# Kernel tuning notes

Hardware: AMD Instinct MI355X
Metric: run time of the kernel (lower is better)

## Reference

```python
import jax, jax.numpy as jnp
import numpy as np

HEADS = 8

def setup_inputs() -> dict:
    key = jax.random.key(0)
    ks = jax.random.split(key, 4)
    b, n, d = 4, 4097, 128  # n = 64*64 + 1 (CLS + spatial)
    x = jax.random.normal(ks[0], (b, n, d), dtype=jnp.float32)
    W_qkv = jax.random.normal(ks[1], (d, 3 * d), dtype=jnp.float32) * (d ** -0.5)
    b_qkv = jnp.zeros((3 * d,), dtype=jnp.float32)
    W_out = jax.random.normal(ks[2], (d, d), dtype=jnp.float32) * (d ** -0.5)
    b_out = jnp.zeros((d,), dtype=jnp.float32)
    return {"x": x, "W_qkv": W_qkv, "b_qkv": b_qkv, "W_out": W_out, "b_out": b_out}

def reference(x, W_qkv, b_qkv, W_out, b_out):
    b, n, d = x.shape
    h = HEADS
    dh = d // h
    scale = d ** -0.5  # note: module scales by dim**-0.5, not head_dim**-0.5
    qkv = x @ W_qkv + b_qkv                      # [b, n, 3d]
    q, k, v = jnp.split(qkv, 3, axis=-1)
    def to_heads(t):
        return t.reshape(b, n, h, dh).transpose(0, 2, 1, 3)  # [b, h, n, dh]
    q, k, v = to_heads(q), to_heads(k), to_heads(v)
    dots = jnp.einsum('bhid,bhjd->bhij', q, k) * scale       # [b, h, n, n]
    attn = jax.nn.softmax(dots, axis=-1)
    out = jnp.einsum('bhij,bhjd->bhid', attn, v)             # [b, h, n, dh]
    out = out.transpose(0, 2, 1, 3).reshape(b, n, d)
    return out @ W_out + b_out
```

## Files before the change

### kernel.cpp

```cpp
#include <hip/hip_runtime.h>
#include <hip/hip_bf16.h>
#include <stdint.h>


#define BB 4
#define NN 4097
#define NNP 4112
#define DD 128
#define HH 8
#define DH 16
#define BH (BB*HH)
#define ROWS (BB*NN)

typedef _Float16 h4 __attribute__((ext_vector_type(4)));
typedef _Float16 h8 __attribute__((ext_vector_type(8)));
typedef __fp16   fp16v2 __attribute__((ext_vector_type(2)));
typedef float    f4 __attribute__((ext_vector_type(4)));

#if __has_builtin(__builtin_amdgcn_exp2f)
#define EXP2F(x) __builtin_amdgcn_exp2f(x)
#else
#define EXP2F(x) exp2f(x)
#endif

union H4u { h4 v; fp16v2 p[2]; };

static __device__ __forceinline__ H4u pack4u(float a, float b, float c, float d) {
    H4u u;
#if __has_builtin(__builtin_amdgcn_cvt_pkrtz)
    u.p[0] = __builtin_amdgcn_cvt_pkrtz(a, b);
    u.p[1] = __builtin_amdgcn_cvt_pkrtz(c, d);
#else
    u.v[0] = (_Float16)a; u.v[1] = (_Float16)b; u.v[2] = (_Float16)c; u.v[3] = (_Float16)d;
#endif
    return u;
}

__global__ __launch_bounds__(384) void qkv_proj(
    const float* __restrict__ x,
    const float* __restrict__ Wqkv,
    const float* __restrict__ bqkv,
    _Float16* __restrict__ Qh,
    _Float16* __restrict__ Kh,
    _Float16* __restrict__ Vh)
{
    const int t  = threadIdx.x;
    const int r0 = blockIdx.x * 4;

    const float bias = bqkv[t];
    float acc0 = bias, acc1 = bias, acc2 = bias, acc3 = bias;

    const float* x0 = x + (size_t)r0 * DD;
    #pragma unroll 4
    for (int k = 0; k < DD; ++k) {
        const float w = Wqkv[k*384 + t];
        acc0 += x0[k]        * w;
        acc1 += x0[DD + k]   * w;
        acc2 += x0[2*DD + k] * w;
        acc3 += x0[3*DD + k] * w;
    }

    const int which = t >> 7, c = t & 127, head = c >> 4, i = c & 15;
    const float QSCALE = 0.08838834764831845f * 1.4426950408889634f;
    _Float16* base = (which == 0) ? Qh : ((which == 1) ? Kh : Vh);
    const float mul = (which == 0) ? QSCALE : 1.0f;

    float accs[4] = {acc0, acc1, acc2, acc3};
    #pragma unroll
    for (int r = 0; r < 4; ++r) {
        const int row  = r0 + r;
        const int bidx = row / NN;
        const int nrow = row - bidx*NN;
        base[(((size_t)(bidx*HH + head))*NNP + nrow)*DH + i] = (_Float16)(accs[r] * mul);
    }
}

__global__ __launch_bounds__(256) void vt_transpose(
    const _Float16* __restrict__ Vh,
    _Float16* __restrict__ Vt)
{
    __shared__ _Float16 tile[128][DH + 2];
    const int tl  = blockIdx.x;
    const int bh  = blockIdx.y;
    const int tid = threadIdx.x;
    const int n0  = tl * 128;
    const int rem = (n0 + 128 <= NNP) ? 128 : (NNP - n0);

    {
        const int r  = tid >> 1;
        const int i8 = (tid & 1) * 8;
        const int rc = (r < rem) ? r : (rem - 1);
        const h8 v = *(const h8*)(Vh + ((size_t)bh*NNP + n0 + rc)*DH + i8);
        #pragma unroll
        for (int j = 0; j < 8; ++j) tile[r][i8 + j] = v[j];
    }
    __syncthreads();
    {
        const int i    = tid >> 4;
        const int nseg = tid & 15;
        if (nseg * 8 < rem) {
            h8 v;
            #pragma unroll
            for (int j = 0; j < 8; ++j) v[j] = tile[nseg*8 + j][i];
            *(h8*)(Vt + ((size_t)bh*DH + i)*NNP + n0 + nseg*8) = v;
        }
    }
}

__global__ __launch_bounds__(256, 8) void attn_mfma(
    const _Float16* __restrict__ Qh,
    const _Float16* __restrict__ Kh,
    const _Float16* __restrict__ Vt,
    _Float16* __restrict__ PACC,
    float* __restrict__ PL)
{
    const int qt   = blockIdx.x;
    const int bh   = blockIdx.y;
    const int sp   = blockIdx.z;
    const int tid  = threadIdx.x;
    const int wave = tid >> 6;
    const int lane = tid & 63;
    const int quad = lane >> 4;
    const int l16  = lane & 15;
    const int bidx = bh >> 3, head = bh & 7;

    const int qbase = qt*256 + wave*64;

    const _Float16* Qb = Qh + (size_t)bh*NNP*DH;
    h4 qf[4];
    #pragma unroll
    for (int g = 0; g < 4; ++g) {
        const int qr = qbase + g*16 + l16;
        const int qc = (qr < NN) ? qr : (NN-1);
        qf[g] = *(const h4*)(Qb + (size_t)qc*DH + quad*4);
    }

    f4 acc[4] = {{0,0,0,0},{0,0,0,0},{0,0,0,0},{0,0,0,0}};
    float ls[4] = {0.f,0.f,0.f,0.f};

    const int t0 = sp*64;
    const int t1 = t0 + 64;

    const _Float16* kp = Kh + ((size_t)bh*NNP + (size_t)t0*16 + l16)*DH + quad*4;
    const _Float16* vp = Vt + ((size_t)bh*DH + l16)*NNP + t0*16 + quad*4;

    h4 ak = *(const h4*)kp;
    h4 av = *(const h4*)vp;
    const f4 zero = {0.f,0.f,0.f,0.f};
#if __has_builtin(__builtin_amdgcn_fdot2)
    const fp16v2 one2 = {(__fp16)1.0f, (__fp16)1.0f};
#endif

    for (int tt = t0; tt < t1; ++tt) {
        kp += 16*DH; vp += 16;
        const h4 nak = *(const h4*)kp;
        const h4 nav = *(const h4*)vp;
        #pragma unroll
        for (int g = 0; g < 4; ++g) {
            f4 d = __builtin_amdgcn_mfma_f32_16x16x16f16(ak, qf[g], zero, 0, 0, 0);
            const float p0 = EXP2F(d[0]), p1 = EXP2F(d[1]), p2 = EXP2F(d[2]), p3 = EXP2F(d[3]);
            const H4u pb = pack4u(p0, p1, p2, p3);
#if __has_builtin(__builtin_amdgcn_fdot2)
            ls[g] = __builtin_amdgcn_fdot2(pb.p[0], one2,
                     __builtin_amdgcn_fdot2(pb.p[1], one2, ls[g], false), false);
#else
            ls[g] += (p0 + p1) + (p2 + p3);
#endif
            acc[g] = __builtin_amdgcn_mfma_f32_16x16x16f16(av, pb.v, acc[g], 0, 0, 0);
        }
        ak = nak; av = nav;
    }

    if (sp == 3) {
        #pragma unroll
        for (int g = 0; g < 4; ++g) {
            f4 d = __builtin_amdgcn_mfma_f32_16x16x16f16(ak, qf[g], zero, 0, 0, 0);
            const float p0 = (quad == 0) ? EXP2F(d[0]) : 0.f;
            ls[g] += p0;
            const H4u pb = pack4u(p0, 0.f, 0.f, 0.f);
            acc[g] = __builtin_amdgcn_mfma_f32_16x16x16f16(av, pb.v, acc[g], 0, 0, 0);
        }
    }

    const size_t rb = (size_t)sp*ROWS + (size_t)bidx*NN;
    #pragma unroll
    for (int g = 0; g < 4; ++g) {
        float l = ls[g];
        l += __shfl_xor(l, 16);
        l += __shfl_xor(l, 32);
        const int qr = qbase + g*16 + l16;
        if (qr < NN) {
            const float inv = 1.0f / l;
            const H4u st = pack4u(acc[g][0]*inv, acc[g][1]*inv, acc[g][2]*inv, acc[g][3]*inv);
            *(h4*)(PACC + (rb + qr)*DD + head*DH + quad*4) = st.v;
            if (quad == 0) PL[(rb + qr)*HH + head] = l;
        }
    }
}

__global__ __launch_bounds__(128) void out_proj_fused(
    const _Float16* __restrict__ PACC,
    const float* __restrict__ PL,
    const float* __restrict__ Wout,
    const float* __restrict__ bout,
    float* __restrict__ out)
{
    __shared__ float lls[256];
    __shared__ float linv[64];
    __shared__ float xr[8*DD];

    const int t  = threadIdx.x;
    const int r0 = blockIdx.x * 8;

    #pragma unroll
    for (int u = 0; u < 2; ++u) {
        const int idx = t + u*128;
        const int sp = idx >> 6, r = (idx >> 3) & 7, h = idx & 7;
        const int row = (r0 + r < ROWS) ? (r0 + r) : (ROWS - 1);
        lls[idx] = PL[((size_t)sp*ROWS + row)*HH + h];
    }
    __syncthreads();
    if (t < 64) {
        const float s = lls[t] + lls[64 + t] + lls[128 + t] + lls[192 + t];
        linv[t] = 1.0f / s;
    }
    __syncthreads();

    const int head = t >> 4;
    #pragma unroll
    for (int r = 0; r < 8; ++r) {
        const int row = (r0 + r < ROWS) ? (r0 + r) : (ROWS - 1);
        float num = 0.f;
        #pragma unroll
        for (int sp = 0; sp < 4; ++sp)
            num += lls[sp*64 + r*8 + head]
                 * (float)PACC[((size_t)sp*ROWS + row)*DD + t];
        xr[r*DD + t] = num * linv[r*8 + head];
    }
    __syncthreads();

    const float bias = bout[t];
    float acc[8];
    #pragma unroll
    for (int r = 0; r < 8; ++r) acc[r] = bias;

    #pragma unroll 4
    for (int k = 0; k < DD; ++k) {
        const float w = Wout[k*DD + t];
        #pragma unroll
        for (int r = 0; r < 8; ++r)
            acc[r] += xr[r*DD + k] * w;
    }

    #pragma unroll
    for (int r = 0; r < 8; ++r) {
        const int row = r0 + r;
        if (row < ROWS) out[(size_t)row*DD + t] = acc[r];
    }
}

extern "C" void kernel_launch(void* const* d_in, const int* in_sizes, int n_in,
                              void* d_out, int out_size, void* d_ws, size_t ws_size,
                              hipStream_t stream) {
    const float* x    = (const float*)d_in[0];
    const float* Wqkv = (const float*)d_in[1];
    const float* bqkv = (const float*)d_in[2];
    const float* Wout = (const float*)d_in[3];
    const float* bout = (const float*)d_in[4];
    for (int i = 0; i < n_in; ++i) {
        switch (in_sizes[i]) {
            case 2097664: x    = (const float*)d_in[i]; break;
            case 49152:   Wqkv = (const float*)d_in[i]; break;
            case 384:     bqkv = (const float*)d_in[i]; break;
            case 16384:   Wout = (const float*)d_in[i]; break;
            case 128:     bout = (const float*)d_in[i]; break;
            default: break;
        }
    }
    float* out = (float*)d_out;

    const size_t perh = (size_t)BH * NNP * DH;
    _Float16* Qh   = (_Float16*)d_ws;
    _Float16* Kh   = Qh + perh;
    _Float16* Vt   = Kh + perh;
    _Float16* Vh   = Vt + perh;
    _Float16* PACC = Vh;
    float*    PL   = (float*)(PACC + (size_t)4*ROWS*DD);

    hipLaunchKernelGGL(qkv_proj, dim3(ROWS/4), dim3(384), 0, stream,
                       x, Wqkv, bqkv, Qh, Kh, Vh);
    hipLaunchKernelGGL(vt_transpose, dim3(33, BH), dim3(256), 0, stream,
                       Vh, Vt);
    hipLaunchKernelGGL(attn_mfma, dim3(17, BH, 4), dim3(256), 0, stream,
                       Qh, Kh, Vt, PACC, PL);
    hipLaunchKernelGGL(out_proj_fused, dim3((ROWS + 7)/8), dim3(128), 0, stream,
                       PACC, PL, Wout, bout, out);
}
```

Before: 203.8 us.

## Run QKV and output projections as fp16 MFMA GEMMs with a prep kernel

A new prep kernel converts x to fp16 and writes transposed fp16 copies of W_qkv (with the Q scale folded in) and W_out. The scalar fp32 QKV and output projection kernels are replaced by wave-level 16x16x16 fp16 MFMA kernels. The output kernel now merges the four split-softmax partials directly into its A fragments. This aims to cut the FP32 ALU cost of the two projections, at the price of an extra conversion pass over x and lower input precision.

```diff
diff --git a/kernel.cpp b/kernel.cpp
--- a/kernel.cpp
+++ b/kernel.cpp
@@ -11,11 +11,14 @@
 #define DH 16
 #define BH (BB*HH)
 #define ROWS (BB*NN)
+#define MT  1025
 
 typedef _Float16 h4 __attribute__((ext_vector_type(4)));
 typedef _Float16 h8 __attribute__((ext_vector_type(8)));
 typedef __fp16   fp16v2 __attribute__((ext_vector_type(2)));
 typedef float    f4 __attribute__((ext_vector_type(4)));
+
+#define QSCALE (0.08838834764831845f * 1.4426950408889634f)
 
 #if __has_builtin(__builtin_amdgcn_exp2f)
 #define EXP2F(x) __builtin_amdgcn_exp2f(x)
@@ -36,42 +39,84 @@
     return u;
 }
 
-__global__ __launch_bounds__(384) void qkv_proj(
+__global__ __launch_bounds__(256) void prep(
     const float* __restrict__ x,
     const float* __restrict__ Wqkv,
+    const float* __restrict__ Wout,
+    _Float16* __restrict__ x16,
+    _Float16* __restrict__ WqkvT,
+    _Float16* __restrict__ WoutT)
+{
+    const int id = blockIdx.x*256 + threadIdx.x;
+    const int NX8 = ROWS*DD/8;
+    if (id < NX8) {
+        const float4* s = (const float4*)(x + (size_t)id*8);
+        const float4 a = s[0], b = s[1];
+        const H4u u0 = pack4u(a.x, a.y, a.z, a.w);
+        const H4u u1 = pack4u(b.x, b.y, b.z, b.w);
+        h4* d = (h4*)(x16 + (size_t)id*8);
+        d[0] = u0.v; d[1] = u1.v;
+    } else if (id < NX8 + 384*128) {
+        const int e = id - NX8;
+        const int n = e >> 7, k = e & 127;
+        const float s = (n < 128) ? QSCALE : 1.0f;
+        WqkvT[e] = (_Float16)(Wqkv[k*384 + n] * s);
+    } else if (id < NX8 + 384*128 + 128*128) {
+        const int e = id - NX8 - 384*128;
+        const int n = e >> 7, k = e & 127;
+        WoutT[e] = (_Float16)(Wout[k*128 + n]);
+    }
+}
+
+__global__ __launch_bounds__(256) void qkv_mfma(
+    const _Float16* __restrict__ x16,
+    const _Float16* __restrict__ WqkvT,
     const float* __restrict__ bqkv,
     _Float16* __restrict__ Qh,
     _Float16* __restrict__ Kh,
     _Float16* __restrict__ Vh)
 {
-    const int t  = threadIdx.x;
-    const int r0 = blockIdx.x * 4;
-
-    const float bias = bqkv[t];
-    float acc0 = bias, acc1 = bias, acc2 = bias, acc3 = bias;
-
-    const float* x0 = x + (size_t)r0 * DD;
-    #pragma unroll 4
-    for (int k = 0; k < DD; ++k) {
-        const float w = Wqkv[k*384 + t];
-        acc0 += x0[k]        * w;
-        acc1 += x0[DD + k]   * w;
-        acc2 += x0[2*DD + k] * w;
-        acc3 += x0[3*DD + k] * w;
-    }
-
-    const int which = t >> 7, c = t & 127, head = c >> 4, i = c & 15;
-    const float QSCALE = 0.08838834764831845f * 1.4426950408889634f;
-    _Float16* base = (which == 0) ? Qh : ((which == 1) ? Kh : Vh);
-    const float mul = (which == 0) ? QSCALE : 1.0f;
-
-    float accs[4] = {acc0, acc1, acc2, acc3};
+    const int wid  = blockIdx.x*4 + (threadIdx.x >> 6);
+    if (wid >= MT) return;
+    const int lane = threadIdx.x & 63;
+    const int quad = lane >> 4, l16 = lane & 15;
+
+    const int arow = wid*16 + l16;
+    const int arc  = (arow < ROWS) ? arow : (ROWS - 1);
+    h4 af[8];
     #pragma unroll
-    for (int r = 0; r < 4; ++r) {
-        const int row  = r0 + r;
-        const int bidx = row / NN;
-        const int nrow = row - bidx*NN;
-        base[(((size_t)(bidx*HH + head))*NNP + nrow)*DH + i] = (_Float16)(accs[r] * mul);
+    for (int kk = 0; kk < 8; ++kk)
+        af[kk] = *(const h4*)(x16 + (size_t)arc*DD + kk*16 + quad*4);
+
+    const int r0 = wid*16 + quad*4;
+
+    for (int nt = 0; nt < 24; nt += 2) {
+        const float b0 = bqkv[nt*16 + l16]      * ((nt   < 8) ? QSCALE : 1.0f);
+        const float b1 = bqkv[nt*16 + 16 + l16] * ((nt+1 < 8) ? QSCALE : 1.0f);
+        f4 a0 = {b0,b0,b0,b0}, a1 = {b1,b1,b1,b1};
+        #pragma unroll
+        for (int kk = 0; kk < 8; ++kk) {
+            const h4 bf0 = *(const h4*)(WqkvT + (size_t)(nt*16     + l16)*DD + kk*16 + quad*4);
+            const h4 bf1 = *(const h4*)(WqkvT + (size_t)(nt*16 + 16 + l16)*DD + kk*16 + quad*4);
+            a0 = __builtin_amdgcn_mfma_f32_16x16x16f16(af[kk], bf0, a0, 0, 0, 0);
+            a1 = __builtin_amdgcn_mfma_f32_16x16x16f16(af[kk], bf1, a1, 0, 0, 0);
+        }
+        #pragma unroll
+        for (int u = 0; u < 2; ++u) {
+            const int ntc = nt + u;
+            const int which = ntc >> 3, head = ntc & 7;
+            _Float16* base = (which == 0) ? Qh : ((which == 1) ? Kh : Vh);
+            const f4 av = u ? a1 : a0;
+            #pragma unroll
+            for (int r = 0; r < 4; ++r) {
+                const int row = r0 + r;
+                if (row < ROWS) {
+                    const int bidx = row / NN;
+                    const int nrow = row - bidx*NN;
+                    base[((size_t)(bidx*HH + head)*NNP + nrow)*DH + l16] = (_Float16)av[r];
+                }
+            }
+        }
     }
 }
 
@@ -198,64 +243,59 @@
     }
 }
 
-__global__ __launch_bounds__(128) void out_proj_fused(
+__global__ __launch_bounds__(256) void out_mfma(
     const _Float16* __restrict__ PACC,
     const float* __restrict__ PL,
-    const float* __restrict__ Wout,
+    const _Float16* __restrict__ WoutT,
     const float* __restrict__ bout,
     float* __restrict__ out)
 {
-    __shared__ float lls[256];
-    __shared__ float linv[64];
-    __shared__ float xr[8*DD];
-
-    const int t  = threadIdx.x;
-    const int r0 = blockIdx.x * 8;
-
+    const int wid  = blockIdx.x*4 + (threadIdx.x >> 6);
+    if (wid >= MT) return;
+    const int lane = threadIdx.x & 63;
+    const int quad = lane >> 4, l16 = lane & 15;
+
+    const int arow = wid*16 + l16;
+    const int arc  = (arow < ROWS) ? arow : (ROWS - 1);
+
+    h4 af[8];
     #pragma unroll
-    for (int u = 0; u < 2; ++u) {
-        const int idx = t + u*128;
-        const int sp = idx >> 6, r = (idx >> 3) & 7, h = idx & 7;
-        const int row = (r0 + r < ROWS) ? (r0 + r) : (ROWS - 1);
-        lls[idx] = PL[((size_t)sp*ROWS + row)*HH + h];
-    }
-    __syncthreads();
-    if (t < 64) {
-        const float s = lls[t] + lls[64 + t] + lls[128 + t] + lls[192 + t];
-        linv[t] = 1.0f / s;
-    }
-    __syncthreads();
-
-    const int head = t >> 4;
-    #pragma unroll
-    for (int r = 0; r < 8; ++r) {
-        const int row = (r0 + r < ROWS) ? (r0 + r) : (ROWS - 1);
-        float num = 0.f;
-        #pragma unroll
-        for (int sp = 0; sp < 4; ++sp)
-            num += lls[sp*64 + r*8 + head]
-                 * (float)PACC[((size_t)sp*ROWS + row)*DD + t];
-        xr[r*DD + t] = num * linv[r*8 + head];
-    }
-    __syncthreads();
-
-    const float bias = bout[t];
-    float acc[8];
-    #pragma unroll
-    for (int r = 0; r < 8; ++r) acc[r] = bias;
-
-    #pragma unroll 4
-    for (int k = 0; k < DD; ++k) {
-        const float w = Wout[k*DD + t];
-        #pragma unroll
-        for (int r = 0; r < 8; ++r)
-            acc[r] += xr[r*DD + k] * w;
-    }
-
-    #pragma unroll
-    for (int r = 0; r < 8; ++r) {
-        const int row = r0 + r;
-        if (row < ROWS) out[(size_t)row*DD + t] = acc[r];
+    for (int kk = 0; kk < 8; ++kk) {
+        float n0 = 0.f, n1 = 0.f, n2 = 0.f, n3 = 0.f, lsum = 0.f;
+        #pragma unroll
+        for (int sp = 0; sp < 4; ++sp) {
+            const float l = PL[((size_t)sp*ROWS + arc)*HH + kk];
+            lsum += l;
+            const h4 p = *(const h4*)(PACC + ((size_t)sp*ROWS + arc)*DD + kk*16 + quad*4);
+            n0 += l*(float)p[0]; n1 += l*(float)p[1];
+            n2 += l*(float)p[2]; n3 += l*(float)p[3];
+        }
+        const float inv = 1.0f / lsum;
+        const H4u u = pack4u(n0*inv, n1*inv, n2*inv, n3*inv);
+        af[kk] = u.v;
+    }
+
+    const int r0 = wid*16 + quad*4;
+
+    for (int nt = 0; nt < 8; nt += 2) {
+        const float b0 = bout[nt*16 + l16];
+        const float b1 = bout[nt*16 + 16 + l16];
+        f4 a0 = {b0,b0,b0,b0}, a1 = {b1,b1,b1,b1};
+        #pragma unroll
+        for (int kk = 0; kk < 8; ++kk) {
+            const h4 bf0 = *(const h4*)(WoutT + (size_t)(nt*16      + l16)*DD + kk*16 + quad*4);
+            const h4 bf1 = *(const h4*)(WoutT + (size_t)(nt*16 + 16 + l16)*DD + kk*16 + quad*4);
+            a0 = __builtin_amdgcn_mfma_f32_16x16x16f16(af[kk], bf0, a0, 0, 0, 0);
+            a1 = __builtin_amdgcn_mfma_f32_16x16x16f16(af[kk], bf1, a1, 0, 0, 0);
+        }
+        #pragma unroll
+        for (int r = 0; r < 4; ++r) {
+            const int row = r0 + r;
+            if (row < ROWS) {
+                out[(size_t)row*DD + nt*16      + l16] = a0[r];
+                out[(size_t)row*DD + nt*16 + 16 + l16] = a1[r];
+            }
+        }
     }
 }
 
@@ -285,14 +325,22 @@
     _Float16* Vt   = Kh + perh;
     _Float16* Vh   = Vt + perh;
     _Float16* PACC = Vh;
-    float*    PL   = (float*)(PACC + (size_t)4*ROWS*DD);
-
-    hipLaunchKernelGGL(qkv_proj, dim3(ROWS/4), dim3(384), 0, stream,
-                       x, Wqkv, bqkv, Qh, Kh, Vh);
+    _Float16* x16  = Vh + perh;
+    float*    PL    = (float*)(PACC + (size_t)4*ROWS*DD);
+    _Float16* WqkvT = (_Float16*)(PL + (size_t)4*ROWS*HH);
+    _Float16* WoutT = WqkvT + 384*128;
+
+    const int NX8 = ROWS*DD/8;
+    const int prep_total = NX8 + 384*128 + 128*128;
+
+    hipLaunchKernelGGL(prep, dim3((prep_total + 255)/256), dim3(256), 0, stream,
+                       x, Wqkv, Wout, x16, WqkvT, WoutT);
+    hipLaunchKernelGGL(qkv_mfma, dim3((MT + 3)/4), dim3(256), 0, stream,
+                       x16, WqkvT, bqkv, Qh, Kh, Vh);
     hipLaunchKernelGGL(vt_transpose, dim3(33, BH), dim3(256), 0, stream,
                        Vh, Vt);
     hipLaunchKernelGGL(attn_mfma, dim3(17, BH, 4), dim3(256), 0, stream,
                        Qh, Kh, Vt, PACC, PL);
-    hipLaunchKernelGGL(out_proj_fused, dim3((ROWS + 7)/8), dim3(128), 0, stream,
-                       PACC, PL, Wout, bout, out);
-}
+    hipLaunchKernelGGL(out_mfma, dim3((MT + 3)/4), dim3(256), 0, stream,
+                       PACC, PL, WoutT, bout, out);
+}
```

Measured after the change: 195.5 us. -4.1%, faster.
